# Performance work log

Measured on AMD Instinct MI355X. Metric: run time of the kernel, lower is better.

## Reference

```python
import jax, jax.numpy as jnp
import numpy as np

VOCAB = 32000
D_MODEL = 1024
D_FF = 4 * D_MODEL
N_LAYERS = 2
N_EXPERTS = 8
TOP_K = 2
BATCH = 4
SEQ = 2048
LN_EPS = 1e-5


def setup_inputs() -> dict:
    key = jax.random.key(0)
    ks = jax.random.split(key, 12)
    s = lambda *dims: 1.0 / np.sqrt(dims[-2] if len(dims) > 1 else dims[-1])
    inp = {
        "tokens": jax.random.randint(ks[0], (BATCH, SEQ), 0, VOCAB, dtype=jnp.int32),
        "symbolic_emb": jax.random.normal(ks[1], (BATCH, D_MODEL), dtype=jnp.float32),
        "emb": jax.random.normal(ks[2], (VOCAB, D_MODEL), dtype=jnp.float32) * 0.02,
        "gate_w": jax.random.normal(ks[3], (N_LAYERS, D_MODEL, N_EXPERTS), dtype=jnp.float32) / np.sqrt(D_MODEL),
        "gate_b": jnp.zeros((N_LAYERS, N_EXPERTS), dtype=jnp.float32),
        "w1": jax.random.normal(ks[4], (N_LAYERS, N_EXPERTS, D_MODEL, D_FF), dtype=jnp.float32) / np.sqrt(D_MODEL),
        "b1": jnp.zeros((N_LAYERS, N_EXPERTS, D_FF), dtype=jnp.float32),
        "w2": jax.random.normal(ks[5], (N_LAYERS, N_EXPERTS, D_FF, D_MODEL), dtype=jnp.float32) / np.sqrt(D_FF),
        "b2": jnp.zeros((N_LAYERS, N_EXPERTS, D_MODEL), dtype=jnp.float32),
        "ln_g": jnp.ones((D_MODEL,), dtype=jnp.float32),
        "ln_b": jnp.zeros((D_MODEL,), dtype=jnp.float32),
    }
    return inp


def _moe_layer(x_flat, gw, gb, w1, b1, w2, b2):
    # x_flat: [T, d]
    probs = jax.nn.softmax(x_flat @ gw + gb, axis=-1)            # [T, E]
    weights, idx = jax.lax.top_k(probs, TOP_K)                   # [T, K]
    # combine weight per (token, expert): sum of top-k weights routed to that expert
    combine = jnp.sum(jax.nn.one_hot(idx, N_EXPERTS, dtype=x_flat.dtype) * weights[..., None], axis=1)  # [T, E]
    out = jnp.zeros_like(x_flat)
    for j in range(N_EXPERTS):  # small fixed structural loop
        h = jax.nn.gelu(x_flat @ w1[j] + b1[j], approximate=False)  # [T, d_ff]
        y = h @ w2[j] + b2[j]                                       # [T, d]
        out = out + combine[:, j:j + 1] * y
    return out


def reference(tokens, symbolic_emb, emb, gate_w, gate_b, w1, b1, w2, b2, ln_g, ln_b):
    x = emb[tokens] + symbolic_emb[:, None, :]                  # [B, S, d]
    T = BATCH * SEQ
    x = x.reshape(T, D_MODEL)
    for l in range(N_LAYERS):
        x = _moe_layer(x, gate_w[l], gate_b[l], w1[l], b1[l], w2[l], b2[l])
    mu = jnp.mean(x, axis=-1, keepdims=True)
    var = jnp.mean(jnp.square(x - mu), axis=-1, keepdims=True)
    x = (x - mu) * jax.lax.rsqrt(var + LN_EPS) * ln_g + ln_b
    return x.reshape(BATCH, SEQ, D_MODEL)
```

## Files before the change

kernel.cpp:

```cpp
#include <hip/hip_runtime.h>
#include <math.h>

#define T_TOK 8192
#define DM 1024
#define DFF 4096
#define NE 8
#define NPAIR 16384
#define MAXTILE 136
#define LN_EPS 1e-5f

typedef __attribute__((ext_vector_type(8))) short bf16x8;
typedef __attribute__((ext_vector_type(4))) float f32x4;
typedef __attribute__((ext_vector_type(4))) unsigned short u16x4;
typedef __attribute__((ext_vector_type(8))) unsigned short u16x8;
typedef unsigned int u32;
typedef unsigned short u16;

__device__ __forceinline__ u16 f2bf(float f) {
  union { float f; u32 u; } v; v.f = f;
  u32 r = (v.u + 0x7fffu + ((v.u >> 16) & 1u)) >> 16;
  return (u16)r;
}
__device__ __forceinline__ float bf2f(u16 h) {
  union { u32 u; float f; } v; v.u = ((u32)h) << 16; return v.f;
}

__device__ __forceinline__ void gll16(const void* g, void* l) {
  __builtin_amdgcn_global_load_lds(
      (const __attribute__((address_space(1))) u32*)g,
      (__attribute__((address_space(3))) u32*)l, 16, 0, 0);
}

__global__ __launch_bounds__(256) void embed_kernel(const int* __restrict__ tok,
    const float* __restrict__ sym, const float* __restrict__ emb,
    float* __restrict__ x, u16* __restrict__ xh, u16* __restrict__ xl)
{
  int t = blockIdx.x;
  int b = t >> 11;
  int tk = tok[t];
  int d = threadIdx.x * 4;
  f32x4 e = *(const f32x4*)(emb + (size_t)tk * DM + d);
  f32x4 s = *(const f32x4*)(sym + (size_t)b * DM + d);
  f32x4 v = e + s;
  *(f32x4*)(x + (size_t)t * DM + d) = v;
  u16x4 hv, lv;
#pragma unroll
  for (int j = 0; j < 4; ++j) {
    u16 hb = f2bf(v[j]);
    hv[j] = hb;
    lv[j] = f2bf(v[j] - bf2f(hb));
  }
  *(u16x4*)(xh + (size_t)t * DM + d) = hv;
  *(u16x4*)(xl + (size_t)t * DM + d) = lv;
}

__global__ __launch_bounds__(256) void gate_kernel(const float* __restrict__ x,
    const float* __restrict__ gw, const float* __restrict__ gb,
    int* __restrict__ topk_idx, float* __restrict__ topk_w)
{
  int lane = threadIdx.x & 63;
  int t = blockIdx.x * 4 + (threadIdx.x >> 6);
  const float* xr = x + (size_t)t * DM;
  double a[8] = {0,0,0,0,0,0,0,0};
  for (int i = 0; i < 16; ++i) {
    int d = i * 64 + lane;
    double xv = (double)xr[d];
    const float* g = gw + (size_t)d * NE;
#pragma unroll
    for (int j = 0; j < 8; ++j) a[j] += xv * (double)g[j];
  }
#pragma unroll
  for (int j = 0; j < 8; ++j) {
#pragma unroll
    for (int sh = 32; sh; sh >>= 1) a[j] += __shfl_xor(a[j], sh);
  }
  if (lane == 0) {
#pragma unroll
    for (int j = 0; j < 8; ++j) a[j] += (double)gb[j];
    double m = a[0];
    for (int j = 1; j < 8; ++j) m = a[j] > m ? a[j] : m;
    double p[8], sum = 0.0;
    for (int j = 0; j < 8; ++j) { p[j] = exp(a[j] - m); sum += p[j]; }
    for (int j = 0; j < 8; ++j) p[j] /= sum;
    int j0 = 0; double b0 = p[0];
    for (int j = 1; j < 8; ++j) if (p[j] > b0) { b0 = p[j]; j0 = j; }
    int j1 = (j0 == 0) ? 1 : 0; double b1v = p[j1];
    for (int j = 0; j < 8; ++j) if (j != j0 && p[j] > b1v) { b1v = p[j]; j1 = j; }
    topk_idx[t*2]   = j0; topk_idx[t*2+1] = j1;
    topk_w[t*2]     = (float)b0; topk_w[t*2+1] = (float)b1v;
  }
}

__global__ __launch_bounds__(256) void count_kernel(const int* __restrict__ topk_idx,
    int* __restrict__ meta)
{
  __shared__ int hist[8];
  int tid = threadIdx.x;
  if (tid < 8) hist[tid] = 0;
  __syncthreads();
  int t = blockIdx.x * 256 + tid;
  atomicAdd(&hist[topk_idx[t*2] & 7], 1);
  atomicAdd(&hist[topk_idx[t*2+1] & 7], 1);
  __syncthreads();
  if (tid < 8) meta[168 + blockIdx.x * 8 + tid] = hist[tid];
}

__global__ __launch_bounds__(64) void scan_kernel(int* __restrict__ meta)
{
  __shared__ int tot[8], off[9], tb[8];
  int lane = threadIdx.x;
  if (lane < 8) {
    int s = 0;
    for (int b = 0; b < 32; ++b) s += meta[168 + b * 8 + lane];
    tot[lane] = s;
  }
  __syncthreads();
  if (lane == 0) {
    int s = 0, nt = 0;
    for (int e = 0; e < 8; ++e) {
      off[e] = s; s += tot[e];
      tb[e] = nt; nt += (tot[e] + 127) >> 7;
    }
    off[8] = s;
    meta[31] = nt;
    for (int i = nt; i < MAXTILE; ++i) meta[32 + i] = -1;
  }
  __syncthreads();
  if (lane < 9) meta[8 + lane] = off[lane];
  if (lane < 8) {
    meta[lane] = tot[lane];
    int n = (tot[lane] + 127) >> 7;
    for (int i = 0; i < n; ++i) meta[32 + tb[lane] + i] = (lane << 16) | i;
    int run = off[lane];
    for (int b = 0; b < 32; ++b) {
      meta[424 + b * 8 + lane] = run;
      run += meta[168 + b * 8 + lane];
    }
  }
}

__global__ __launch_bounds__(256) void scatter_kernel(int* __restrict__ topk_idx,
    const int* __restrict__ meta, int* __restrict__ pair_token)
{
  __shared__ int hist[8];
  __shared__ int base[8];
  int tid = threadIdx.x;
  if (tid < 8) { hist[tid] = 0; base[tid] = meta[424 + blockIdx.x * 8 + tid]; }
  __syncthreads();
  int t = blockIdx.x * 256 + tid;
#pragma unroll
  for (int k = 0; k < 2; ++k) {
    int e = topk_idx[t*2 + k] & 7;
    int pos = atomicAdd(&hist[e], 1);
    int slot = base[e] + pos;
    pair_token[slot] = t;
    topk_idx[t*2 + k] = e | (slot << 3);
  }
}

template<bool LO>
__global__ __launch_bounds__(256) void transpose_kernel(const float* __restrict__ src,
    u16* __restrict__ dsth, u16* __restrict__ dstl, int K, int N)
{
  __shared__ float tile[64][65];
  int e = blockIdx.z;
  const float* s = src + (size_t)e * K * N;
  size_t dbase = (size_t)e * K * N;
  int n0 = blockIdx.x * 64, k0 = blockIdx.y * 64;
  int tid = threadIdx.x;
  int nl = tid & 63;
  int kq = tid >> 6;
#pragma unroll
  for (int j = 0; j < 16; ++j) {
    int kl = j * 4 + kq;
    tile[nl][kl] = s[(size_t)(k0 + kl) * N + n0 + nl];
  }
  __syncthreads();
#pragma unroll
  for (int it = 0; it < 2; ++it) {
    int task = it * 256 + tid;
    int nr = task >> 3;
    int ch = task & 7;
    u16x8 oh, ol;
#pragma unroll
    for (int j = 0; j < 8; ++j) {
      float v = tile[nr][ch*8 + j];
      u16 hb = f2bf(v);
      oh[j] = hb;
      if (LO) ol[j] = f2bf(v - bf2f(hb));
    }
    size_t doff = dbase + (size_t)(n0 + nr) * K + k0 + ch*8;
    *(u16x8*)(dsth + doff) = oh;
    if (LO) *(u16x8*)(dstl + doff) = ol;
  }
}

__global__ __launch_bounds__(256) void w2g_kernel(const float* __restrict__ w2,
    const float* __restrict__ gw, float* __restrict__ w2g)
{
  int wid = blockIdx.x * 4 + (threadIdx.x >> 6);
  int lane = threadIdx.x & 63;
  int e = wid >> 12, f = wid & 4095;
  const float* row = w2 + ((size_t)e * DFF + f) * DM;
  float a0=0,a1=0,a2=0,a3=0,a4=0,a5=0,a6=0,a7=0;
  for (int i = 0; i < 4; ++i) {
    int d0 = i * 256 + lane * 4;
    f32x4 xv = *(const f32x4*)(row + d0);
#pragma unroll
    for (int q = 0; q < 4; ++q) {
      const f32x4* gr = (const f32x4*)(gw + (size_t)(d0 + q) * 8);
      f32x4 g0 = gr[0], g1 = gr[1];
      float xq = xv[q];
      a0 += xq*g0.x; a1 += xq*g0.y; a2 += xq*g0.z; a3 += xq*g0.w;
      a4 += xq*g1.x; a5 += xq*g1.y; a6 += xq*g1.z; a7 += xq*g1.w;
    }
  }
  float acc[8] = {a0,a1,a2,a3,a4,a5,a6,a7};
#pragma unroll
  for (int j = 0; j < 8; ++j) {
#pragma unroll
    for (int sh = 32; sh; sh >>= 1) acc[j] += __shfl_xor(acc[j], sh);
  }
  if (lane == 0) {
#pragma unroll
    for (int j = 0; j < 8; ++j) w2g[(size_t)wid * 8 + j] = acc[j];
  }
}

__global__ __launch_bounds__(256) void b2g_kernel(const float* __restrict__ b2,
    const float* __restrict__ gw, float* __restrict__ b2g)
{
  int w = blockIdx.x * 4 + (threadIdx.x >> 6);
  int lane = threadIdx.x & 63;
  int e = w >> 3, j = w & 7;
  float acc = 0.f;
  for (int i = 0; i < 16; ++i) {
    int d = i * 64 + lane;
    acc += b2[(size_t)e * DM + d] * gw[(size_t)d * 8 + j];
  }
#pragma unroll
  for (int sh = 32; sh; sh >>= 1) acc += __shfl_xor(acc, sh);
  if (lane == 0) b2g[w] = acc;
}

__global__ __launch_bounds__(256) void pairlogit_kernel(const u16* __restrict__ hh,
    const u16* __restrict__ hl, const int* __restrict__ off,
    const float* __restrict__ w2g, float* __restrict__ R)
{
  int p = blockIdx.x * 4 + (threadIdx.x >> 6);
  int lane = threadIdx.x & 63;
  int e = 0;
#pragma unroll
  for (int j = 1; j < 8; ++j) e += (p >= off[j]) ? 1 : 0;
  const float* wg = w2g + (size_t)e * DFF * 8;
  const u16* ph = hh + (size_t)p * DFF;
  const u16* pl = hl + (size_t)p * DFF;
  float a0=0,a1=0,a2=0,a3=0,a4=0,a5=0,a6=0,a7=0;
  for (int i = 0; i < 8; ++i) {
    int f0 = i * 512 + lane * 8;
    u16x8 vh = *(const u16x8*)(ph + f0);
    u16x8 vl = *(const u16x8*)(pl + f0);
#pragma unroll
    for (int q = 0; q < 8; ++q) {
      float hv = bf2f(vh[q]) + bf2f(vl[q]);
      const f32x4* wr = (const f32x4*)(wg + (size_t)(f0 + q) * 8);
      f32x4 g0 = wr[0], g1 = wr[1];
      a0 += hv*g0.x; a1 += hv*g0.y; a2 += hv*g0.z; a3 += hv*g0.w;
      a4 += hv*g1.x; a5 += hv*g1.y; a6 += hv*g1.z; a7 += hv*g1.w;
    }
  }
  float acc[8] = {a0,a1,a2,a3,a4,a5,a6,a7};
#pragma unroll
  for (int j = 0; j < 8; ++j) {
#pragma unroll
    for (int sh = 32; sh; sh >>= 1) acc[j] += __shfl_xor(acc[j], sh);
  }
  if (lane == 0) {
#pragma unroll
    for (int j = 0; j < 8; ++j) R[(size_t)p * 8 + j] = acc[j];
  }
}

__global__ __launch_bounds__(256) void gate1_kernel(const float* __restrict__ R,
    const float* __restrict__ b2g, const float* __restrict__ gb,
    int* __restrict__ topk_idx, float* __restrict__ topk_w)
{
  int t = blockIdx.x * 256 + threadIdx.x;
  int v0 = topk_idx[t*2], v1 = topk_idx[t*2+1];
  int e0 = v0 & 7, e1 = v1 & 7;
  int s0 = v0 >> 3, s1 = v1 >> 3;
  double w0 = (double)topk_w[t*2], w1 = (double)topk_w[t*2+1];
  double a[8];
#pragma unroll
  for (int j = 0; j < 8; ++j)
    a[j] = w0 * ((double)R[(size_t)s0*8+j] + (double)b2g[e0*8+j])
         + w1 * ((double)R[(size_t)s1*8+j] + (double)b2g[e1*8+j])
         + (double)gb[j];
  double m = a[0];
  for (int j = 1; j < 8; ++j) m = a[j] > m ? a[j] : m;
  double p[8], sum = 0.0;
  for (int j = 0; j < 8; ++j) { p[j] = exp(a[j] - m); sum += p[j]; }
  for (int j = 0; j < 8; ++j) p[j] /= sum;
  int j0 = 0; double b0 = p[0];
  for (int j = 1; j < 8; ++j) if (p[j] > b0) { b0 = p[j]; j0 = j; }
  int j1 = (j0 == 0) ? 1 : 0; double b1v = p[j1];
  for (int j = 0; j < 8; ++j) if (j != j0 && p[j] > b1v) { b1v = p[j]; j1 = j; }
  topk_idx[t*2]   = j0; topk_idx[t*2+1] = j1;
  topk_w[t*2]     = (float)b0; topk_w[t*2+1] = (float)b1v;
}

template<int K0, int NSEG, int NTOT, bool GATHER, int MODE>
__global__ __launch_bounds__(256, 4) void gemm128_kernel(
    const u16* __restrict__ Ah, const u16* __restrict__ Al,
    const u16* __restrict__ Bh, const u16* __restrict__ Bl,
    const float* __restrict__ bias, const int* __restrict__ off,
    const int* __restrict__ tiletab, const int* __restrict__ pair_token,
    u16* __restrict__ outh, u16* __restrict__ outl, float* __restrict__ outy)
{
  constexpr int NT = (K0 * NSEG) / 32;
  const int tt = tiletab[blockIdx.y];
  if (tt < 0) return;
  const int e  = tt >> 16;
  const int mt = tt & 0xffff;
  const int off_e = off[e], off_e1 = off[e + 1];
  const int p0 = off_e + mt * 128;
  const int NX = gridDim.x;
  int bx = blockIdx.x;
  int ntile = ((NX & 7) == 0) ? ((bx & 7) * (NX >> 3) + (bx >> 3)) : bx;
  const int n0 = ntile * 128;

  __shared__ __align__(16) u16 AL[2][4096];
  __shared__ __align__(16) u16 BL[2][4096];

  const int tid  = threadIdx.x;
  const int lane = tid & 63;
  const int wave = tid >> 6;
  const int wm = wave >> 1, wn = wave & 1;
  const int wbase = tid & 192;

  size_t aoff[2], boff[2];
#pragma unroll
  for (int i = 0; i < 2; ++i) {
    int c = i * 256 + tid;
    int r = c >> 2;
    int cs = (c & 3) ^ ((r >> 1) & 3);
    int idx = p0 + r;
    if (idx >= off_e1) idx = p0;
    int ar = GATHER ? pair_token[idx] : idx;
    aoff[i] = (size_t)ar * K0 + (size_t)(cs * 8);
    boff[i] = ((size_t)e * NTOT + n0 + r) * K0 + (size_t)(cs * 8);
  }

  auto stage = [&](int b, int t) {
    int kk = t * 32;
    int seg = (NSEG == 3) ? (kk >> 10) : 0;
    int kc  = (NSEG == 3) ? (kk & (K0 - 1)) : kk;
    const u16* abase = ((NSEG == 3 && seg == 1) ? Al : Ah) + kc;
    const u16* bbase = ((NSEG == 3 && seg == 2) ? Bl : Bh) + kc;
#pragma unroll
    for (int i = 0; i < 2; ++i) {
      int cb = i * 256 + wbase;
      gll16(abase + aoff[i], &AL[b][cb * 8]);
      gll16(bbase + boff[i], &BL[b][cb * 8]);
    }
  };

  f32x4 acc[4][4];
  const f32x4 fzero = {0.f, 0.f, 0.f, 0.f};
#pragma unroll
  for (int m = 0; m < 4; ++m)
#pragma unroll
    for (int n = 0; n < 4; ++n) acc[m][n] = fzero;

  stage(0, 0);
  __syncthreads();

  int buf = 0;
  for (int t = 0; t < NT; ++t) {
    if (t + 1 < NT) stage(buf ^ 1, t + 1);
    bf16x8 af[4], bf[4];
#pragma unroll
    for (int m = 0; m < 4; ++m) {
      int row = wm * 64 + m * 16 + (lane & 15);
      af[m] = *(const bf16x8*)&AL[buf][row * 32 + (((lane >> 4) ^ ((row >> 1) & 3)) << 3)];
    }
#pragma unroll
    for (int n = 0; n < 4; ++n) {
      int row = wn * 64 + n * 16 + (lane & 15);
      bf[n] = *(const bf16x8*)&BL[buf][row * 32 + (((lane >> 4) ^ ((row >> 1) & 3)) << 3)];
    }
    __builtin_amdgcn_s_setprio(1);
#pragma unroll
    for (int m = 0; m < 4; ++m)
#pragma unroll
      for (int n = 0; n < 4; ++n)
        acc[m][n] = __builtin_amdgcn_mfma_f32_16x16x32_bf16(af[m], bf[n], acc[m][n], 0, 0, 0);
    __builtin_amdgcn_s_setprio(0);
    __syncthreads();
    buf ^= 1;
  }

  float bv[4];
#pragma unroll
  for (int n = 0; n < 4; ++n)
    bv[n] = bias[(size_t)e * NTOT + n0 + wn * 64 + n * 16 + (lane & 15)];

#pragma unroll
  for (int m = 0; m < 4; ++m) {
    int rbase = p0 + wm * 64 + m * 16 + ((lane >> 4) << 2);
#pragma unroll
    for (int n = 0; n < 4; ++n) {
      int col = n0 + wn * 64 + n * 16 + (lane & 15);
#pragma unroll
      for (int r = 0; r < 4; ++r) {
        int rowp = rbase + r;
        if (rowp < off_e1) {
          float v = acc[m][n][r] + bv[n];
          if constexpr (MODE <= 1) {
            v = 0.5f * v * (1.0f + erff(v * 0.70710678118654752f));
            u16 hb = f2bf(v);
            outh[(size_t)rowp * NTOT + col] = hb;
            if constexpr (MODE == 1)
              outl[(size_t)rowp * NTOT + col] = f2bf(v - bf2f(hb));
          } else {
            outy[(size_t)rowp * NTOT + col] = v;
          }
        }
      }
    }
  }
}

__global__ __launch_bounds__(256) void combine0_kernel(const float* __restrict__ y,
    const int* __restrict__ topk_idx, const float* __restrict__ topk_w,
    u16* __restrict__ xh)
{
  int t = blockIdx.x;
  int d = threadIdx.x * 4;
  int s0 = topk_idx[t*2] >> 3, s1 = topk_idx[t*2 + 1] >> 3;
  float w0 = topk_w[t*2], w1 = topk_w[t*2 + 1];
  f32x4 y0 = *(const f32x4*)(y + (size_t)s0 * DM + d);
  f32x4 y1 = *(const f32x4*)(y + (size_t)s1 * DM + d);
  f32x4 v = y0 * w0 + y1 * w1;
  u16x4 hv;
#pragma unroll
  for (int j = 0; j < 4; ++j) hv[j] = f2bf(v[j]);
  *(u16x4*)(xh + (size_t)t * DM + d) = hv;
}

__global__ __launch_bounds__(256) void combine1_ln_kernel(const float* __restrict__ y,
    const int* __restrict__ topk_idx, const float* __restrict__ topk_w,
    const float* __restrict__ g, const float* __restrict__ b, float* __restrict__ out)
{
  int t = blockIdx.x;
  int d = threadIdx.x * 4;
  int s0 = topk_idx[t*2] >> 3, s1 = topk_idx[t*2 + 1] >> 3;
  float w0 = topk_w[t*2], w1 = topk_w[t*2 + 1];
  f32x4 y0 = *(const f32x4*)(y + (size_t)s0 * DM + d);
  f32x4 y1 = *(const f32x4*)(y + (size_t)s1 * DM + d);
  f32x4 v = y0 * w0 + y1 * w1;
  float s = v.x + v.y + v.z + v.w;
  float sq = v.x*v.x + v.y*v.y + v.z*v.z + v.w*v.w;
#pragma unroll
  for (int sh = 32; sh; sh >>= 1) { s += __shfl_xor(s, sh); sq += __shfl_xor(sq, sh); }
  __shared__ float red[8];
  int wave = threadIdx.x >> 6, lane = threadIdx.x & 63;
  if (lane == 0) { red[wave] = s; red[4 + wave] = sq; }
  __syncthreads();
  s = red[0] + red[1] + red[2] + red[3];
  sq = red[4] + red[5] + red[6] + red[7];
  float mu = s * (1.0f / DM);
  float var = sq * (1.0f / DM) - mu * mu;
  float inv = rsqrtf(var + LN_EPS);
  f32x4 gv = *(const f32x4*)(g + d);
  f32x4 bv = *(const f32x4*)(b + d);
  f32x4 o;
  o.x = (v.x - mu) * inv * gv.x + bv.x;
  o.y = (v.y - mu) * inv * gv.y + bv.y;
  o.z = (v.z - mu) * inv * gv.z + bv.z;
  o.w = (v.w - mu) * inv * gv.w + bv.w;
  *(f32x4*)(out + (size_t)t * DM + d) = o;
}

extern "C" void kernel_launch(void* const* d_in, const int* in_sizes, int n_in,
                              void* d_out, int out_size, void* d_ws, size_t ws_size,
                              hipStream_t stream)
{
  const int*   tokens = (const int*)d_in[0];
  const float* sym    = (const float*)d_in[1];
  const float* emb    = (const float*)d_in[2];
  const float* gate_w = (const float*)d_in[3];
  const float* gate_b = (const float*)d_in[4];
  const float* w1     = (const float*)d_in[5];
  const float* b1     = (const float*)d_in[6];
  const float* w2     = (const float*)d_in[7];
  const float* b2     = (const float*)d_in[8];
  const float* ln_g   = (const float*)d_in[9];
  const float* ln_b   = (const float*)d_in[10];

  char* ws = (char*)d_ws;
  float* x   = (float*)(ws);
  u16*   xh  = (u16*)  (ws + 33554432);
  u16*   xl  = (u16*)  (ws + 50331648);
  u16*   hh  = (u16*)  (ws + 67108864);
  u16*   hl  = (u16*)  (ws + 201326592);
  float* y   = (float*)(ws + 201326592);
  u16*   wTh = (u16*)  (ws + 335544320);
  u16*   wTl = (u16*)  (ws + 402653184);
  float* W2G = (float*)(ws + 402653184);
  float* R   = (float*)(ws + 403701760);
  float* B2G = (float*)(ws + 404226048);
  int*   pair_token = (int*)  (ws + 469762048);
  int*   topk_idx   = (int*)  (ws + 469893120);
  float* topk_w     = (float*)(ws + 469958656);
  int*   meta       = (int*)  (ws + 470024192);

  embed_kernel<<<T_TOK, 256, 0, stream>>>(tokens, sym, emb, x, xh, xl);

  gate_kernel<<<T_TOK / 4, 256, 0, stream>>>(x, gate_w, gate_b, topk_idx, topk_w);
  count_kernel<<<T_TOK / 256, 256, 0, stream>>>(topk_idx, meta);
  scan_kernel<<<1, 64, 0, stream>>>(meta);
  scatter_kernel<<<T_TOK / 256, 256, 0, stream>>>(topk_idx, meta, pair_token);

  transpose_kernel<true><<<dim3(DFF / 64, DM / 64, NE), 256, 0, stream>>>(
      w1, wTh, wTl, DM, DFF);
  gemm128_kernel<DM, 3, DFF, true, 1><<<dim3(DFF / 128, MAXTILE), 256, 0, stream>>>(
      xh, xl, wTh, wTl, b1, meta + 8, meta + 32, pair_token, hh, hl, nullptr);

  w2g_kernel<<<NE * DFF / 4, 256, 0, stream>>>(w2, gate_w + (size_t)DM * NE, W2G);
  b2g_kernel<<<16, 256, 0, stream>>>(b2, gate_w + (size_t)DM * NE, B2G);
  pairlogit_kernel<<<NPAIR / 4, 256, 0, stream>>>(hh, hl, meta + 8, W2G, R);

  transpose_kernel<false><<<dim3(DM / 64, DFF / 64, NE), 256, 0, stream>>>(
      w2, wTh, wTl, DFF, DM);
  gemm128_kernel<DFF, 1, DM, false, 2><<<dim3(DM / 128, MAXTILE), 256, 0, stream>>>(
      hh, nullptr, wTh, nullptr, b2, meta + 8, meta + 32, pair_token,
      nullptr, nullptr, y);

  combine0_kernel<<<T_TOK, 256, 0, stream>>>(y, topk_idx, topk_w, xh);

  gate1_kernel<<<T_TOK / 256, 256, 0, stream>>>(R, B2G, gate_b + NE,
                                                topk_idx, topk_w);
  count_kernel<<<T_TOK / 256, 256, 0, stream>>>(topk_idx, meta);
  scan_kernel<<<1, 64, 0, stream>>>(meta);
  scatter_kernel<<<T_TOK / 256, 256, 0, stream>>>(topk_idx, meta, pair_token);

  transpose_kernel<false><<<dim3(DFF / 64, DM / 64, NE), 256, 0, stream>>>(
      w1 + (size_t)NE * DM * DFF, wTh, wTl, DM, DFF);
  gemm128_kernel<DM, 1, DFF, true, 0><<<dim3(DFF / 128, MAXTILE), 256, 0, stream>>>(
      xh, nullptr, wTh, nullptr, b1 + (size_t)NE * DFF, meta + 8, meta + 32,
      pair_token, hh, nullptr, nullptr);

  transpose_kernel<false><<<dim3(DM / 64, DFF / 64, NE), 256, 0, stream>>>(
      w2 + (size_t)NE * DFF * DM, wTh, wTl, DFF, DM);
  gemm128_kernel<DFF, 1, DM, false, 2><<<dim3(DM / 128, MAXTILE), 256, 0, stream>>>(
      hh, nullptr, wTh, nullptr, b2 + (size_t)NE * DM, meta + 8, meta + 32,
      pair_token, nullptr, nullptr, y);

  combine1_ln_kernel<<<T_TOK, 256, 0, stream>>>(y, topk_idx, topk_w,
                                                ln_g, ln_b, (float*)d_out);
}
```

Before: 1.873 ms.

## Switch expert GEMMs to 256x256 tiles with 8-wave split-K pipelined staging

Replaces the 128x128 grouped expert GEMM with a 256x256 tile kernel using 512 threads (8 waves, each 128x64). K-steps of 64 are split into two 32-wide halves, with a finer-grained schedule that interleaves LDS reads, async global-to-LDS loads and MFMA blocks under explicit vmcnt waits and barriers. The aim is more data reuse per loaded byte and better latency hiding. In exchange it uses more registers and LDS per block, and with 256-row expert tiles there is more padding waste and fewer blocks, which risks under-filling the GPU.

Result: no change. 1.907 ms (+1.8%).

```diff
diff --git a/kernel.cpp b/kernel.cpp
--- a/kernel.cpp
+++ b/kernel.cpp
@@ -6,7 +6,7 @@
 #define DFF 4096
 #define NE 8
 #define NPAIR 16384
-#define MAXTILE 136
+#define MAXTILE 72
 #define LN_EPS 1e-5f
 
 typedef __attribute__((ext_vector_type(8))) short bf16x8;
@@ -119,7 +119,7 @@
     int s = 0, nt = 0;
     for (int e = 0; e < 8; ++e) {
       off[e] = s; s += tot[e];
-      tb[e] = nt; nt += (tot[e] + 127) >> 7;
+      tb[e] = nt; nt += (tot[e] + 255) >> 8;
     }
     off[8] = s;
     meta[31] = nt;
@@ -129,7 +129,7 @@
   if (lane < 9) meta[8 + lane] = off[lane];
   if (lane < 8) {
     meta[lane] = tot[lane];
-    int n = (tot[lane] + 127) >> 7;
+    int n = (tot[lane] + 255) >> 8;
     for (int i = 0; i < n; ++i) meta[32 + tb[lane] + i] = (lane << 16) | i;
     int run = off[lane];
     for (int b = 0; b < 32; ++b) {
@@ -310,38 +310,40 @@
 }
 
 template<int K0, int NSEG, int NTOT, bool GATHER, int MODE>
-__global__ __launch_bounds__(256, 4) void gemm128_kernel(
+__global__ __launch_bounds__(512, 2) void gemm256_kernel(
     const u16* __restrict__ Ah, const u16* __restrict__ Al,
     const u16* __restrict__ Bh, const u16* __restrict__ Bl,
     const float* __restrict__ bias, const int* __restrict__ off,
     const int* __restrict__ tiletab, const int* __restrict__ pair_token,
     u16* __restrict__ outh, u16* __restrict__ outl, float* __restrict__ outy)
 {
-  constexpr int NT = (K0 * NSEG) / 32;
+  constexpr int NT = (K0 * NSEG) / 64;
+  static_assert(NT >= 2, "");
   const int tt = tiletab[blockIdx.y];
   if (tt < 0) return;
   const int e  = tt >> 16;
   const int mt = tt & 0xffff;
   const int off_e = off[e], off_e1 = off[e + 1];
-  const int p0 = off_e + mt * 128;
+  const int p0 = off_e + mt * 256;
   const int NX = gridDim.x;
   int bx = blockIdx.x;
   int ntile = ((NX & 7) == 0) ? ((bx & 7) * (NX >> 3) + (bx >> 3)) : bx;
-  const int n0 = ntile * 128;
-
-  __shared__ __align__(16) u16 AL[2][4096];
-  __shared__ __align__(16) u16 BL[2][4096];
+  const int n0 = ntile * 256;
+
+  __shared__ __align__(16) u16 ALs[2][2][8192];
+  __shared__ __align__(16) u16 BLs[2][2][8192];
 
   const int tid  = threadIdx.x;
   const int lane = tid & 63;
   const int wave = tid >> 6;
-  const int wm = wave >> 1, wn = wave & 1;
-  const int wbase = tid & 192;
+  const int wm = wave >> 2;
+  const int wn = wave & 3;
+  const int wbase = tid & 448;
 
   size_t aoff[2], boff[2];
 #pragma unroll
   for (int i = 0; i < 2; ++i) {
-    int c = i * 256 + tid;
+    int c = i * 512 + tid;
     int r = c >> 2;
     int cs = (c & 3) ^ ((r >> 1) & 3);
     int idx = p0 + r;
@@ -351,71 +353,122 @@
     boff[i] = ((size_t)e * NTOT + n0 + r) * K0 + (size_t)(cs * 8);
   }
 
-  auto stage = [&](int b, int t) {
-    int kk = t * 32;
+  auto stageA = [&](int t, int kh) {
+    int kk = t * 64 + kh * 32;
     int seg = (NSEG == 3) ? (kk >> 10) : 0;
     int kc  = (NSEG == 3) ? (kk & (K0 - 1)) : kk;
-    const u16* abase = ((NSEG == 3 && seg == 1) ? Al : Ah) + kc;
-    const u16* bbase = ((NSEG == 3 && seg == 2) ? Bl : Bh) + kc;
-#pragma unroll
-    for (int i = 0; i < 2; ++i) {
-      int cb = i * 256 + wbase;
-      gll16(abase + aoff[i], &AL[b][cb * 8]);
-      gll16(bbase + boff[i], &BL[b][cb * 8]);
-    }
+    const u16* base = (NSEG == 3 && seg == 1) ? Al : Ah;
+    u16* dst = &ALs[t & 1][kh][0];
+#pragma unroll
+    for (int i = 0; i < 2; ++i)
+      gll16(base + aoff[i] + kc, dst + (i * 512 + wbase) * 8);
   };
-
-  f32x4 acc[4][4];
+  auto stageB = [&](int t, int kh) {
+    int kk = t * 64 + kh * 32;
+    int seg = (NSEG == 3) ? (kk >> 10) : 0;
+    int kc  = (NSEG == 3) ? (kk & (K0 - 1)) : kk;
+    const u16* base = (NSEG == 3 && seg == 2) ? Bl : Bh;
+    u16* dst = &BLs[t & 1][kh][0];
+#pragma unroll
+    for (int i = 0; i < 2; ++i)
+      gll16(base + boff[i] + kc, dst + (i * 512 + wbase) * 8);
+  };
+
+  f32x4 acc[8][4];
   const f32x4 fzero = {0.f, 0.f, 0.f, 0.f};
 #pragma unroll
-  for (int m = 0; m < 4; ++m)
+  for (int m = 0; m < 8; ++m)
 #pragma unroll
     for (int n = 0; n < 4; ++n) acc[m][n] = fzero;
 
-  stage(0, 0);
-  __syncthreads();
-
-  int buf = 0;
+  auto rdA4 = [&](bf16x8* dst, int par, int kh, int mbase) {
+    const u16* L = &ALs[par][kh][0];
+#pragma unroll
+    for (int mf = 0; mf < 4; ++mf) {
+      int row = wm * 128 + (mbase + mf) * 16 + (lane & 15);
+      dst[mf] = *(const bf16x8*)&L[row * 32 + (((lane >> 4) ^ ((row >> 1) & 3)) << 3)];
+    }
+  };
+  auto rdB4 = [&](bf16x8* dst, int par, int kh) {
+    const u16* L = &BLs[par][kh][0];
+#pragma unroll
+    for (int nf = 0; nf < 4; ++nf) {
+      int row = wn * 64 + nf * 16 + (lane & 15);
+      dst[nf] = *(const bf16x8*)&L[row * 32 + (((lane >> 4) ^ ((row >> 1) & 3)) << 3)];
+    }
+  };
+
+#define MMBLK(MB, A4, B4)                                                        \
+  {                                                                              \
+    __builtin_amdgcn_s_setprio(1);                                               \
+    _Pragma("unroll")                                                            \
+    for (int mf = 0; mf < 4; ++mf)                                               \
+      _Pragma("unroll")                                                          \
+      for (int nf = 0; nf < 4; ++nf)                                             \
+        acc[(MB) + mf][nf] = __builtin_amdgcn_mfma_f32_16x16x32_bf16(            \
+            (A4)[mf], (B4)[nf], acc[(MB) + mf][nf], 0, 0, 0);                    \
+    __builtin_amdgcn_s_setprio(0);                                               \
+  }
+
+  stageA(0, 0); stageB(0, 0);
+  stageA(0, 1); stageB(0, 1);
+  stageA(1, 0); stageB(1, 0);
+  asm volatile("s_waitcnt vmcnt(8)" ::: "memory");
+  __builtin_amdgcn_s_barrier();
+  asm volatile("" ::: "memory");
+
   for (int t = 0; t < NT; ++t) {
-    if (t + 1 < NT) stage(buf ^ 1, t + 1);
-    bf16x8 af[4], bf[4];
-#pragma unroll
-    for (int m = 0; m < 4; ++m) {
-      int row = wm * 64 + m * 16 + (lane & 15);
-      af[m] = *(const bf16x8*)&AL[buf][row * 32 + (((lane >> 4) ^ ((row >> 1) & 3)) << 3)];
-    }
-#pragma unroll
-    for (int n = 0; n < 4; ++n) {
-      int row = wn * 64 + n * 16 + (lane & 15);
-      bf[n] = *(const bf16x8*)&BL[buf][row * 32 + (((lane >> 4) ^ ((row >> 1) & 3)) << 3)];
-    }
-    __builtin_amdgcn_s_setprio(1);
-#pragma unroll
-    for (int m = 0; m < 4; ++m)
-#pragma unroll
-      for (int n = 0; n < 4; ++n)
-        acc[m][n] = __builtin_amdgcn_mfma_f32_16x16x32_bf16(af[m], bf[n], acc[m][n], 0, 0, 0);
-    __builtin_amdgcn_s_setprio(0);
-    __syncthreads();
-    buf ^= 1;
-  }
+    const int par = t & 1;
+    bf16x8 bA[4], aA[4], aB[4], bC[4], aC[4], aD[4];
+    rdB4(bA, par, 0);
+    rdA4(aA, par, 0, 0);
+    if (t + 1 < NT) stageA(t + 1, 1);
+    __builtin_amdgcn_s_barrier();
+    MMBLK(0, aA, bA);
+    __builtin_amdgcn_s_barrier();
+    rdA4(aB, par, 0, 4);
+    if (t + 1 < NT) stageB(t + 1, 1);
+    __builtin_amdgcn_s_barrier();
+    MMBLK(4, aB, bA);
+    if (t + 1 < NT) { asm volatile("s_waitcnt vmcnt(8)" ::: "memory"); }
+    else            { asm volatile("s_waitcnt vmcnt(0)" ::: "memory"); }
+    __builtin_amdgcn_s_barrier();
+    asm volatile("" ::: "memory");
+    rdB4(bC, par, 1);
+    rdA4(aC, par, 1, 0);
+    if (t + 2 < NT) stageA(t + 2, 0);
+    __builtin_amdgcn_s_barrier();
+    MMBLK(0, aC, bC);
+    __builtin_amdgcn_s_barrier();
+    rdA4(aD, par, 1, 4);
+    if (t + 2 < NT) stageB(t + 2, 0);
+    __builtin_amdgcn_s_barrier();
+    MMBLK(4, aD, bC);
+    if (t + 1 < NT) {
+      if (t + 2 < NT) { asm volatile("s_waitcnt vmcnt(8)" ::: "memory"); }
+      else            { asm volatile("s_waitcnt vmcnt(4)" ::: "memory"); }
+      __builtin_amdgcn_s_barrier();
+      asm volatile("" ::: "memory");
+    }
+  }
+#undef MMBLK
 
   float bv[4];
 #pragma unroll
-  for (int n = 0; n < 4; ++n)
-    bv[n] = bias[(size_t)e * NTOT + n0 + wn * 64 + n * 16 + (lane & 15)];
-
-#pragma unroll
-  for (int m = 0; m < 4; ++m) {
-    int rbase = p0 + wm * 64 + m * 16 + ((lane >> 4) << 2);
-#pragma unroll
-    for (int n = 0; n < 4; ++n) {
-      int col = n0 + wn * 64 + n * 16 + (lane & 15);
+  for (int nf = 0; nf < 4; ++nf)
+    bv[nf] = bias[(size_t)e * NTOT + n0 + wn * 64 + nf * 16 + (lane & 15)];
+
+#pragma unroll
+  for (int mf = 0; mf < 8; ++mf) {
+    int rbase = p0 + wm * 128 + mf * 16 + ((lane >> 4) << 2);
+#pragma unroll
+    for (int nf = 0; nf < 4; ++nf) {
+      int col = n0 + wn * 64 + nf * 16 + (lane & 15);
 #pragma unroll
       for (int r = 0; r < 4; ++r) {
         int rowp = rbase + r;
         if (rowp < off_e1) {
-          float v = acc[m][n][r] + bv[n];
+          float v = acc[mf][nf][r] + bv[nf];
           if constexpr (MODE <= 1) {
             v = 0.5f * v * (1.0f + erff(v * 0.70710678118654752f));
             u16 hb = f2bf(v);
@@ -524,7 +577,7 @@
 
   transpose_kernel<true><<<dim3(DFF / 64, DM / 64, NE), 256, 0, stream>>>(
       w1, wTh, wTl, DM, DFF);
-  gemm128_kernel<DM, 3, DFF, true, 1><<<dim3(DFF / 128, MAXTILE), 256, 0, stream>>>(
+  gemm256_kernel<DM, 3, DFF, true, 1><<<dim3(DFF / 256, MAXTILE), 512, 0, stream>>>(
       xh, xl, wTh, wTl, b1, meta + 8, meta + 32, pair_token, hh, hl, nullptr);
 
   w2g_kernel<<<NE * DFF / 4, 256, 0, stream>>>(w2, gate_w + (size_t)DM * NE, W2G);
@@ -533,7 +586,7 @@
 
   transpose_kernel<false><<<dim3(DM / 64, DFF / 64, NE), 256, 0, stream>>>(
       w2, wTh, wTl, DFF, DM);
-  gemm128_kernel<DFF, 1, DM, false, 2><<<dim3(DM / 128, MAXTILE), 256, 0, stream>>>(
+  gemm256_kernel<DFF, 1, DM, false, 2><<<dim3(DM / 256, MAXTILE), 512, 0, stream>>>(
       hh, nullptr, wTh, nullptr, b2, meta + 8, meta + 32, pair_token,
       nullptr, nullptr, y);
 
@@ -547,13 +600,13 @@
 
   transpose_kernel<false><<<dim3(DFF / 64, DM / 64, NE), 256, 0, stream>>>(
       w1 + (size_t)NE * DM * DFF, wTh, wTl, DM, DFF);
-  gemm128_kernel<DM, 1, DFF, true, 0><<<dim3(DFF / 128, MAXTILE), 256, 0, stream>>>(
+  gemm256_kernel<DM, 1, DFF, true, 0><<<dim3(DFF / 256, MAXTILE), 512, 0, stream>>>(
       xh, nullptr, wTh, nullptr, b1 + (size_t)NE * DFF, meta + 8, meta + 32,
       pair_token, hh, nullptr, nullptr);
 
   transpose_kernel<false><<<dim3(DM / 64, DFF / 64, NE), 256, 0, stream>>>(
       w2 + (size_t)NE * DFF * DM, wTh, wTl, DFF, DM);
-  gemm128_kernel<DFF, 1, DM, false, 2><<<dim3(DM / 128, MAXTILE), 256, 0, stream>>>(
+  gemm256_kernel<DFF, 1, DM, false, 2><<<dim3(DM / 256, MAXTILE), 512, 0, stream>>>(
       hh, nullptr, wTh, nullptr, b2 + (size_t)NE * DM, meta + 8, meta + 32,
       pair_token, nullptr, nullptr, y);
 
```
